# Optimization experiments

Measured on AMD Instinct MI355X. Metric: run time of the kernel, lower is better.

## Reference

```python
import jax, jax.numpy as jnp
import numpy as np

D = 1024  # input_dim


def setup_inputs() -> dict:
    key = jax.random.key(0)
    ks = jax.random.split(key, 7)
    s = 1.0 / np.sqrt(D)
    x = jax.random.normal(ks[0], (4, 2048, D), dtype=jnp.float32)
    Wq = jax.random.uniform(ks[1], (D, D), jnp.float32, -s, s)
    bq = jax.random.uniform(ks[2], (D,), jnp.float32, -s, s)
    Wk = jax.random.uniform(ks[3], (D, D), jnp.float32, -s, s)
    bk = jax.random.uniform(ks[4], (D,), jnp.float32, -s, s)
    Wv = jax.random.uniform(ks[5], (D, D), jnp.float32, -s, s)
    bv = jax.random.uniform(ks[6], (D,), jnp.float32, -s, s)
    return {"x": x, "Wq": Wq, "bq": bq, "Wk": Wk, "bk": bk, "Wv": Wv, "bv": bv}


def reference(x, Wq, bq, Wk, bk, Wv, bv):
    # nn.Linear: x @ W.T + b
    q = jnp.einsum('bsd,ed->bse', x, Wq) + bq
    k = jnp.einsum('bsd,ed->bse', x, Wk) + bk
    v = jnp.einsum('bsd,ed->bse', x, Wv) + bv
    scale = 1.0 / jnp.sqrt(jnp.asarray(x.shape[-1], x.dtype))
    scores = jnp.einsum('bqe,bke->bqk', q, k) * scale  # [B,S,S]
    weights = jax.nn.softmax(scores, axis=-1)
    return jnp.einsum('bqk,bke->bqe', weights, v)
```

## Files before the change

kernel.cpp:

```cpp
#include <hip/hip_runtime.h>
#include <hip/hip_bf16.h>
#include <stdint.h>


typedef float f32x4 __attribute__((ext_vector_type(4)));
typedef short s16x8 __attribute__((ext_vector_type(8)));

__device__ __forceinline__ uint16_t f2bf(float f) {
    uint32_t u = __float_as_uint(f);
    u += 0x7fffu + ((u >> 16) & 1u);
    return (uint16_t)(u >> 16);
}

#define GLOAD16(gp, lp)                                                  \
    __builtin_amdgcn_global_load_lds(                                    \
        (const __attribute__((address_space(1))) uint32_t*)(gp),         \
        (__attribute__((address_space(3))) uint32_t*)(lp), 16, 0, 0)


__global__ __launch_bounds__(256, 2) void proj_qkv(
    const uint16_t* __restrict__ xb, const uint16_t* __restrict__ wqb,
    const uint16_t* __restrict__ wkb, const uint16_t* __restrict__ wvb,
    const float* __restrict__ bq, const float* __restrict__ bk,
    const float* __restrict__ bv,
    uint16_t* __restrict__ qb, uint16_t* __restrict__ kb,
    uint16_t* __restrict__ vtb)
{
    __shared__ __attribute__((aligned(16))) uint16_t As[128 * 64];
    __shared__ __attribute__((aligned(16))) uint16_t Bs1[128 * 64];
    __shared__ __attribute__((aligned(16))) uint16_t Bs2[128 * 64];

    const int id = blockIdx.x;
    const bool qk = id < 512;

    const int t = threadIdx.x;
    const int wave = t >> 6, lane = t & 63;
    const int wm = (wave >> 1) * 64, wn = (wave & 1) * 64;
    const int lr = lane & 15;
    const int lr7 = lr & 7;

    long long row0, col0;
    const uint16_t *A, *B1, *B2;
    if (qk) {
        row0 = (long long)(id >> 3) * 128;
        col0 = (long long)(id & 7) * 128;
        A = xb; B1 = wqb; B2 = wkb;
    } else {
        const int vid = id - 512;
        row0 = (long long)(vid & 7) * 128;
        col0 = (long long)(vid >> 3) * 128;
        A = wvb; B1 = xb; B2 = nullptr;
    }

    const uint16_t* gA[4]; const uint16_t* gB1[4]; const uint16_t* gB2[4];
    uint16_t* lA[4]; uint16_t* lB1[4]; uint16_t* lB2[4];
#pragma unroll
    for (int p = 0; p < 4; ++p) {
        const int cs = p * 256 + wave * 64 + lane;
        const int rr = cs >> 3;
        const int kc = ((cs & 7) ^ (rr & 7)) * 8;
        gA[p]  = A  + (row0 + rr) * 1024 + kc;
        gB1[p] = B1 + (col0 + rr) * 1024 + kc;
        if (qk) gB2[p] = B2 + (col0 + rr) * 1024 + kc;
        lA[p]  = As  + (p * 256 + wave * 64) * 8;
        lB1[p] = Bs1 + (p * 256 + wave * 64) * 8;
        lB2[p] = Bs2 + (p * 256 + wave * 64) * 8;
    }

    f32x4 acc1[4][4] = {};
    f32x4 acc2[4][4] = {};

    for (int k0 = 0; k0 < 1024; k0 += 64) {
#pragma unroll
        for (int p = 0; p < 4; ++p) GLOAD16(gA[p] + k0, lA[p]);
#pragma unroll
        for (int p = 0; p < 4; ++p) GLOAD16(gB1[p] + k0, lB1[p]);
        if (qk) {
#pragma unroll
            for (int p = 0; p < 4; ++p) GLOAD16(gB2[p] + k0, lB2[p]);
        }
        __syncthreads();

#pragma unroll
        for (int kk = 0; kk < 2; ++kk) {
            const int lka = ((kk * 4 + (lane >> 4)) ^ lr7) * 8;
            s16x8 a[4], b[4];
#pragma unroll
            for (int i = 0; i < 4; ++i)
                a[i] = *(const s16x8*)(As + (wm + i * 16 + lr) * 64 + lka);
#pragma unroll
            for (int j = 0; j < 4; ++j)
                b[j] = *(const s16x8*)(Bs1 + (wn + j * 16 + lr) * 64 + lka);
#pragma unroll
            for (int i = 0; i < 4; ++i)
#pragma unroll
                for (int j = 0; j < 4; ++j)
                    acc1[i][j] = __builtin_amdgcn_mfma_f32_16x16x32_bf16(
                        a[i], b[j], acc1[i][j], 0, 0, 0);
            if (qk) {
#pragma unroll
                for (int j = 0; j < 4; ++j)
                    b[j] = *(const s16x8*)(Bs2 + (wn + j * 16 + lr) * 64 + lka);
#pragma unroll
                for (int i = 0; i < 4; ++i)
#pragma unroll
                    for (int j = 0; j < 4; ++j)
                        acc2[i][j] = __builtin_amdgcn_mfma_f32_16x16x32_bf16(
                            a[i], b[j], acc2[i][j], 0, 0, 0);
            }
        }
        __syncthreads();
    }

    const int rbase = wm + (lane >> 4) * 4;
    const int cbase = wn + lr;
    if (qk) {
#pragma unroll
        for (int i = 0; i < 4; ++i)
#pragma unroll
            for (int rr = 0; rr < 4; ++rr) {
                const long long row = row0 + rbase + i * 16 + rr;
#pragma unroll
                for (int j = 0; j < 4; ++j) {
                    const long long col = col0 + cbase + j * 16;
                    qb[row * 1024 + col] = f2bf((acc1[i][j][rr] + bq[col]) * 0.03125f);
                    kb[row * 1024 + col] = f2bf(acc2[i][j][rr] + bk[col]);
                }
            }
    } else {
#pragma unroll
        for (int i = 0; i < 4; ++i)
#pragma unroll
            for (int rr = 0; rr < 4; ++rr) {
                const long long row = row0 + rbase + i * 16 + rr;
                const float bb = bv[row];
#pragma unroll
                for (int j = 0; j < 4; ++j) {
                    const long long col = col0 + cbase + j * 16;
                    vtb[row * 8192 + col] = f2bf(acc1[i][j][rr] + bb);
                }
            }
    }
}

__global__ __launch_bounds__(256, 2) void gemm_exp(
    const uint16_t* __restrict__ Q, const uint16_t* __restrict__ Km,
    uint16_t* __restrict__ P, float* __restrict__ sums)
{
    __shared__ __attribute__((aligned(16))) uint16_t As[128 * 64];
    __shared__ __attribute__((aligned(16))) uint16_t Bs1[128 * 64];
    __shared__ __attribute__((aligned(16))) uint16_t Bs2[128 * 64];

    const int z = blockIdx.z;
    const uint16_t* Ab = Q  + (long long)z * 2048 * 1024;
    const uint16_t* Bb = Km + (long long)z * 2048 * 1024;
    uint16_t* Cb = P + (long long)z * 2048 * 2048;
    float* ax = sums + (long long)z * 2048;

    const int t = threadIdx.x;
    const int wave = t >> 6, lane = t & 63;
    const int wm = (wave >> 1) * 64, wn = (wave & 1) * 64;
    const int lr = lane & 15;
    const int lr7 = lr & 7;
    const long long row0  = (long long)blockIdx.x * 128;
    const long long col0a = (long long)blockIdx.y * 256;
    const long long col0b = col0a + 128;

    const uint16_t* gA[4]; const uint16_t* gB1[4]; const uint16_t* gB2[4];
    uint16_t* lA[4]; uint16_t* lB1[4]; uint16_t* lB2[4];
#pragma unroll
    for (int p = 0; p < 4; ++p) {
        const int cs = p * 256 + wave * 64 + lane;
        const int rr = cs >> 3;
        const int kc = ((cs & 7) ^ (rr & 7)) * 8;
        gA[p]  = Ab + (row0  + rr) * 1024 + kc;
        gB1[p] = Bb + (col0a + rr) * 1024 + kc;
        gB2[p] = Bb + (col0b + rr) * 1024 + kc;
        lA[p]  = As  + (p * 256 + wave * 64) * 8;
        lB1[p] = Bs1 + (p * 256 + wave * 64) * 8;
        lB2[p] = Bs2 + (p * 256 + wave * 64) * 8;
    }

    f32x4 acc1[4][4] = {};
    f32x4 acc2[4][4] = {};

    for (int k0 = 0; k0 < 1024; k0 += 64) {
#pragma unroll
        for (int p = 0; p < 4; ++p) GLOAD16(gA[p] + k0, lA[p]);
#pragma unroll
        for (int p = 0; p < 4; ++p) GLOAD16(gB1[p] + k0, lB1[p]);
#pragma unroll
        for (int p = 0; p < 4; ++p) GLOAD16(gB2[p] + k0, lB2[p]);
        __syncthreads();

#pragma unroll
        for (int kk = 0; kk < 2; ++kk) {
            const int lka = ((kk * 4 + (lane >> 4)) ^ lr7) * 8;
            s16x8 a[4], b[4];
#pragma unroll
            for (int i = 0; i < 4; ++i)
                a[i] = *(const s16x8*)(As + (wm + i * 16 + lr) * 64 + lka);
#pragma unroll
            for (int j = 0; j < 4; ++j)
                b[j] = *(const s16x8*)(Bs1 + (wn + j * 16 + lr) * 64 + lka);
#pragma unroll
            for (int i = 0; i < 4; ++i)
#pragma unroll
                for (int j = 0; j < 4; ++j)
                    acc1[i][j] = __builtin_amdgcn_mfma_f32_16x16x32_bf16(
                        a[i], b[j], acc1[i][j], 0, 0, 0);
#pragma unroll
            for (int j = 0; j < 4; ++j)
                b[j] = *(const s16x8*)(Bs2 + (wn + j * 16 + lr) * 64 + lka);
#pragma unroll
            for (int i = 0; i < 4; ++i)
#pragma unroll
                for (int j = 0; j < 4; ++j)
                    acc2[i][j] = __builtin_amdgcn_mfma_f32_16x16x32_bf16(
                        a[i], b[j], acc2[i][j], 0, 0, 0);
        }
        __syncthreads();
    }

    const int rbase = wm + (lane >> 4) * 4;
    const int cbase = wn + lr;
#pragma unroll
    for (int i = 0; i < 4; ++i)
#pragma unroll
        for (int rr = 0; rr < 4; ++rr) {
            const long long row = row0 + rbase + i * 16 + rr;
            float s = 0.f;
#pragma unroll
            for (int j = 0; j < 4; ++j) {
                const long long ca = col0a + cbase + j * 16;
                const long long cb2 = col0b + cbase + j * 16;
                const float va = __expf(acc1[i][j][rr]);
                const float vb = __expf(acc2[i][j][rr]);
                Cb[row * 2048 + ca]  = f2bf(va);
                Cb[row * 2048 + cb2] = f2bf(vb);
                s += va + vb;
            }
            s += __shfl_xor(s, 1);
            s += __shfl_xor(s, 2);
            s += __shfl_xor(s, 4);
            s += __shfl_xor(s, 8);
            if (lr == 0) atomicAdd(&ax[row], s);
        }
}

__global__ __launch_bounds__(256, 2) void gemm_pv(
    const uint16_t* __restrict__ P, const uint16_t* __restrict__ Vt,
    float* __restrict__ Out, const float* __restrict__ sums)
{
    __shared__ __attribute__((aligned(16))) uint16_t As[128 * 64];
    __shared__ __attribute__((aligned(16))) uint16_t Bs[128 * 64];

    const int z = blockIdx.z;
    const uint16_t* Ab = P + (long long)z * 2048 * 2048;
    const uint16_t* Bb = Vt + (long long)z * 2048;
    float* Cb = Out + (long long)z * 2048 * 1024;
    const float* ax = sums + (long long)z * 2048;

    const int t = threadIdx.x;
    const int wave = t >> 6, lane = t & 63;
    const int wm = (wave >> 1) * 64, wn = (wave & 1) * 64;
    const int lr = lane & 15;
    const int lr7 = lr & 7;
    const long long row0 = (long long)blockIdx.x * 128;
    const long long col0 = (long long)blockIdx.y * 128;

    const uint16_t* gA[4]; const uint16_t* gB[4];
    uint16_t* lA[4]; uint16_t* lB[4];
#pragma unroll
    for (int p = 0; p < 4; ++p) {
        const int cs = p * 256 + wave * 64 + lane;
        const int rr = cs >> 3;
        const int kc = ((cs & 7) ^ (rr & 7)) * 8;
        gA[p] = Ab + (row0 + rr) * 2048 + kc;
        gB[p] = Bb + (col0 + rr) * 8192 + kc;
        lA[p] = As + (p * 256 + wave * 64) * 8;
        lB[p] = Bs + (p * 256 + wave * 64) * 8;
    }

    f32x4 acc[4][4] = {};

    for (int k0 = 0; k0 < 2048; k0 += 64) {
#pragma unroll
        for (int p = 0; p < 4; ++p) GLOAD16(gA[p] + k0, lA[p]);
#pragma unroll
        for (int p = 0; p < 4; ++p) GLOAD16(gB[p] + k0, lB[p]);
        __syncthreads();

#pragma unroll
        for (int kk = 0; kk < 2; ++kk) {
            const int lka = ((kk * 4 + (lane >> 4)) ^ lr7) * 8;
            s16x8 a[4], b[4];
#pragma unroll
            for (int i = 0; i < 4; ++i)
                a[i] = *(const s16x8*)(As + (wm + i * 16 + lr) * 64 + lka);
#pragma unroll
            for (int j = 0; j < 4; ++j)
                b[j] = *(const s16x8*)(Bs + (wn + j * 16 + lr) * 64 + lka);
#pragma unroll
            for (int i = 0; i < 4; ++i)
#pragma unroll
                for (int j = 0; j < 4; ++j)
                    acc[i][j] = __builtin_amdgcn_mfma_f32_16x16x32_bf16(
                        a[i], b[j], acc[i][j], 0, 0, 0);
        }
        __syncthreads();
    }

    const int rbase = wm + (lane >> 4) * 4;
    const int cbase = wn + lr;
#pragma unroll
    for (int i = 0; i < 4; ++i)
#pragma unroll
        for (int rr = 0; rr < 4; ++rr) {
            const long long row = row0 + rbase + i * 16 + rr;
            const float linv = __builtin_amdgcn_rcpf(ax[row]);
#pragma unroll
            for (int j = 0; j < 4; ++j) {
                const long long col = col0 + cbase + j * 16;
                Cb[row * 1024 + col] = acc[i][j][rr] * linv;
            }
        }
}

__global__ void cast_all(const float* __restrict__ x, const float* __restrict__ Wq,
                         const float* __restrict__ Wk, const float* __restrict__ Wv,
                         uint16_t* __restrict__ xb, uint16_t* __restrict__ wqb,
                         uint16_t* __restrict__ wkb, uint16_t* __restrict__ wvb,
                         float* __restrict__ sums) {
    const int b = blockIdx.x;
    const float* in;
    uint16_t* out;
    int i;
    if (b < 8192)       { in = x;  out = xb;  i = b * 256 + threadIdx.x; }
    else if (b < 9216)  { in = Wq; out = wqb; i = (b - 8192) * 256 + threadIdx.x; }
    else if (b < 10240) { in = Wk; out = wkb; i = (b - 9216) * 256 + threadIdx.x; }
    else if (b < 11264) { in = Wv; out = wvb; i = (b - 10240) * 256 + threadIdx.x; }
    else {
        int j = (b - 11264) * 256 + threadIdx.x;
        ((float4*)sums)[j] = make_float4(0.f, 0.f, 0.f, 0.f);
        return;
    }
    float4 v = ((const float4*)in)[i];
    ushort4 o = make_ushort4(f2bf(v.x), f2bf(v.y), f2bf(v.z), f2bf(v.w));
    ((ushort4*)out)[i] = o;
}

extern "C" void kernel_launch(void* const* d_in, const int* in_sizes, int n_in,
                              void* d_out, int out_size, void* d_ws, size_t ws_size,
                              hipStream_t stream) {
    const float* x  = (const float*)d_in[0];
    const float* Wq = (const float*)d_in[1];
    const float* bq = (const float*)d_in[2];
    const float* Wk = (const float*)d_in[3];
    const float* bk = (const float*)d_in[4];
    const float* Wv = (const float*)d_in[5];
    const float* bv = (const float*)d_in[6];

    uint8_t* w = (uint8_t*)d_ws;
    uint16_t* xb  = (uint16_t*)w; w += (size_t)8192 * 1024 * 2;
    uint16_t* wqb = (uint16_t*)w; w += (size_t)1024 * 1024 * 2;
    uint16_t* wkb = (uint16_t*)w; w += (size_t)1024 * 1024 * 2;
    uint16_t* wvb = (uint16_t*)w; w += (size_t)1024 * 1024 * 2;
    uint16_t* qb  = (uint16_t*)w; w += (size_t)8192 * 1024 * 2;
    uint16_t* kb  = (uint16_t*)w; w += (size_t)8192 * 1024 * 2;
    uint16_t* vtb = (uint16_t*)w; w += (size_t)8192 * 1024 * 2;
    uint16_t* pb  = (uint16_t*)w; w += (size_t)4 * 2048 * 2048 * 2;
    float*    sums = (float*)w;  w += (size_t)8192 * 4;

    cast_all<<<dim3(11272), dim3(256), 0, stream>>>(x, Wq, Wk, Wv,
                                                    xb, wqb, wkb, wvb, sums);
    proj_qkv<<<dim3(1024), 256, 0, stream>>>(xb, wqb, wkb, wvb, bq, bk, bv,
                                             qb, kb, vtb);
    gemm_exp<<<dim3(16, 8, 4), 256, 0, stream>>>(qb, kb, pb, sums);
    gemm_pv<<<dim3(16, 8, 4), 256, 0, stream>>>(pb, vtb, (float*)d_out, sums);
}
```

Baseline: 234.6 us.

## Shrink proj K-tile, remap block order for L2 locality, raise occupancy bounds

The projection kernel's K-tile shrinks from 64 to 32, which halves its LDS use and changes the swizzle and load pattern, and its launch bound rises to 3 blocks per CU. The QK-exp and PV kernels switch to a 1D grid with a grouped block mapping, so neighbouring blocks share A and B tiles in L2, and their launch bounds rise to 3 and 4. The aim is more resident blocks to hide latency and fewer redundant global fetches. The cost is twice as many barriers per K step in the projection, and possible register spilling under the tighter bounds.

```diff
diff --git a/kernel.cpp b/kernel.cpp
--- a/kernel.cpp
+++ b/kernel.cpp
@@ -18,7 +18,7 @@
         (__attribute__((address_space(3))) uint32_t*)(lp), 16, 0, 0)
 
 
-__global__ __launch_bounds__(256, 2) void proj_qkv(
+__global__ __launch_bounds__(256, 3) void proj_qkv(
     const uint16_t* __restrict__ xb, const uint16_t* __restrict__ wqb,
     const uint16_t* __restrict__ wkb, const uint16_t* __restrict__ wvb,
     const float* __restrict__ bq, const float* __restrict__ bk,
@@ -26,9 +26,9 @@
     uint16_t* __restrict__ qb, uint16_t* __restrict__ kb,
     uint16_t* __restrict__ vtb)
 {
-    __shared__ __attribute__((aligned(16))) uint16_t As[128 * 64];
-    __shared__ __attribute__((aligned(16))) uint16_t Bs1[128 * 64];
-    __shared__ __attribute__((aligned(16))) uint16_t Bs2[128 * 64];
+    __shared__ __attribute__((aligned(16))) uint16_t As[128 * 32];
+    __shared__ __attribute__((aligned(16))) uint16_t Bs1[128 * 32];
+    __shared__ __attribute__((aligned(16))) uint16_t Bs2[128 * 32];
 
     const int id = blockIdx.x;
     const bool qk = id < 512;
@@ -37,77 +37,80 @@
     const int wave = t >> 6, lane = t & 63;
     const int wm = (wave >> 1) * 64, wn = (wave & 1) * 64;
     const int lr = lane & 15;
-    const int lr7 = lr & 7;
 
     long long row0, col0;
     const uint16_t *A, *B1, *B2;
     if (qk) {
-        row0 = (long long)(id >> 3) * 128;
-        col0 = (long long)(id & 7) * 128;
+        const int m = ((id >> 6) << 3) + (id & 7);
+        const int n = (id >> 3) & 7;
+        row0 = (long long)m * 128;
+        col0 = (long long)n * 128;
         A = xb; B1 = wqb; B2 = wkb;
     } else {
         const int vid = id - 512;
-        row0 = (long long)(vid & 7) * 128;
-        col0 = (long long)(vid >> 3) * 128;
+        const int m = (vid >> 3) & 7;
+        const int n = (vid & 7) + ((vid >> 6) << 3);
+        row0 = (long long)m * 128;
+        col0 = (long long)n * 128;
         A = wvb; B1 = xb; B2 = nullptr;
     }
 
-    const uint16_t* gA[4]; const uint16_t* gB1[4]; const uint16_t* gB2[4];
-    uint16_t* lA[4]; uint16_t* lB1[4]; uint16_t* lB2[4];
-#pragma unroll
-    for (int p = 0; p < 4; ++p) {
-        const int cs = p * 256 + wave * 64 + lane;
-        const int rr = cs >> 3;
-        const int kc = ((cs & 7) ^ (rr & 7)) * 8;
-        gA[p]  = A  + (row0 + rr) * 1024 + kc;
-        gB1[p] = B1 + (col0 + rr) * 1024 + kc;
-        if (qk) gB2[p] = B2 + (col0 + rr) * 1024 + kc;
-        lA[p]  = As  + (p * 256 + wave * 64) * 8;
-        lB1[p] = Bs1 + (p * 256 + wave * 64) * 8;
-        lB2[p] = Bs2 + (p * 256 + wave * 64) * 8;
-    }
+    const int c0 = wave * 64 + lane;
+    const int c1 = c0 + 256;
+    const int kc0 = ((c0 & 3) ^ ((c0 >> 3) & 3)) * 8;
+    const int kc1 = ((c1 & 3) ^ ((c1 >> 3) & 3)) * 8;
+    const uint16_t* gA0  = A  + (row0 + (c0 >> 2)) * 1024 + kc0;
+    const uint16_t* gA1  = A  + (row0 + (c1 >> 2)) * 1024 + kc1;
+    const uint16_t* gB10 = B1 + (col0 + (c0 >> 2)) * 1024 + kc0;
+    const uint16_t* gB11 = B1 + (col0 + (c1 >> 2)) * 1024 + kc1;
+    const uint16_t* gB20 = qk ? B2 + (col0 + (c0 >> 2)) * 1024 + kc0 : nullptr;
+    const uint16_t* gB21 = qk ? B2 + (col0 + (c1 >> 2)) * 1024 + kc1 : nullptr;
+    uint16_t* lA0  = As  + wave * 512;
+    uint16_t* lA1  = As  + wave * 512 + 2048;
+    uint16_t* lB10 = Bs1 + wave * 512;
+    uint16_t* lB11 = Bs1 + wave * 512 + 2048;
+    uint16_t* lB20 = Bs2 + wave * 512;
+    uint16_t* lB21 = Bs2 + wave * 512 + 2048;
+
+    const int lka = (((lane >> 4) ^ ((lr >> 1) & 3))) * 8;
 
     f32x4 acc1[4][4] = {};
     f32x4 acc2[4][4] = {};
 
-    for (int k0 = 0; k0 < 1024; k0 += 64) {
-#pragma unroll
-        for (int p = 0; p < 4; ++p) GLOAD16(gA[p] + k0, lA[p]);
-#pragma unroll
-        for (int p = 0; p < 4; ++p) GLOAD16(gB1[p] + k0, lB1[p]);
+    for (int k0 = 0; k0 < 1024; k0 += 32) {
+        GLOAD16(gA0 + k0, lA0);
+        GLOAD16(gA1 + k0, lA1);
+        GLOAD16(gB10 + k0, lB10);
+        GLOAD16(gB11 + k0, lB11);
         if (qk) {
-#pragma unroll
-            for (int p = 0; p < 4; ++p) GLOAD16(gB2[p] + k0, lB2[p]);
-        }
-        __syncthreads();
-
-#pragma unroll
-        for (int kk = 0; kk < 2; ++kk) {
-            const int lka = ((kk * 4 + (lane >> 4)) ^ lr7) * 8;
-            s16x8 a[4], b[4];
-#pragma unroll
-            for (int i = 0; i < 4; ++i)
-                a[i] = *(const s16x8*)(As + (wm + i * 16 + lr) * 64 + lka);
-#pragma unroll
-            for (int j = 0; j < 4; ++j)
-                b[j] = *(const s16x8*)(Bs1 + (wn + j * 16 + lr) * 64 + lka);
+            GLOAD16(gB20 + k0, lB20);
+            GLOAD16(gB21 + k0, lB21);
+        }
+        __syncthreads();
+
+        s16x8 a[4], b[4];
+#pragma unroll
+        for (int i = 0; i < 4; ++i)
+            a[i] = *(const s16x8*)(As + (wm + i * 16 + lr) * 32 + lka);
+#pragma unroll
+        for (int j = 0; j < 4; ++j)
+            b[j] = *(const s16x8*)(Bs1 + (wn + j * 16 + lr) * 32 + lka);
+#pragma unroll
+        for (int i = 0; i < 4; ++i)
+#pragma unroll
+            for (int j = 0; j < 4; ++j)
+                acc1[i][j] = __builtin_amdgcn_mfma_f32_16x16x32_bf16(
+                    a[i], b[j], acc1[i][j], 0, 0, 0);
+        if (qk) {
+#pragma unroll
+            for (int j = 0; j < 4; ++j)
+                b[j] = *(const s16x8*)(Bs2 + (wn + j * 16 + lr) * 32 + lka);
 #pragma unroll
             for (int i = 0; i < 4; ++i)
 #pragma unroll
                 for (int j = 0; j < 4; ++j)
-                    acc1[i][j] = __builtin_amdgcn_mfma_f32_16x16x32_bf16(
-                        a[i], b[j], acc1[i][j], 0, 0, 0);
-            if (qk) {
-#pragma unroll
-                for (int j = 0; j < 4; ++j)
-                    b[j] = *(const s16x8*)(Bs2 + (wn + j * 16 + lr) * 64 + lka);
-#pragma unroll
-                for (int i = 0; i < 4; ++i)
-#pragma unroll
-                    for (int j = 0; j < 4; ++j)
-                        acc2[i][j] = __builtin_amdgcn_mfma_f32_16x16x32_bf16(
-                            a[i], b[j], acc2[i][j], 0, 0, 0);
-            }
+                    acc2[i][j] = __builtin_amdgcn_mfma_f32_16x16x32_bf16(
+                        a[i], b[j], acc2[i][j], 0, 0, 0);
         }
         __syncthreads();
     }
@@ -143,7 +146,7 @@
     }
 }
 
-__global__ __launch_bounds__(256, 2) void gemm_exp(
+__global__ __launch_bounds__(256, 3) void gemm_exp(
     const uint16_t* __restrict__ Q, const uint16_t* __restrict__ Km,
     uint16_t* __restrict__ P, float* __restrict__ sums)
 {
@@ -151,7 +154,11 @@
     __shared__ __attribute__((aligned(16))) uint16_t Bs1[128 * 64];
     __shared__ __attribute__((aligned(16))) uint16_t Bs2[128 * 64];
 
-    const int z = blockIdx.z;
+    const int id = blockIdx.x;
+    const int g = (id & 7) + ((id >> 6) << 3);
+    const int y = (id >> 3) & 7;
+    const int xblk = g & 15, z = g >> 4;
+
     const uint16_t* Ab = Q  + (long long)z * 2048 * 1024;
     const uint16_t* Bb = Km + (long long)z * 2048 * 1024;
     uint16_t* Cb = P + (long long)z * 2048 * 2048;
@@ -162,8 +169,8 @@
     const int wm = (wave >> 1) * 64, wn = (wave & 1) * 64;
     const int lr = lane & 15;
     const int lr7 = lr & 7;
-    const long long row0  = (long long)blockIdx.x * 128;
-    const long long col0a = (long long)blockIdx.y * 256;
+    const long long row0  = (long long)xblk * 128;
+    const long long col0a = (long long)y * 256;
     const long long col0b = col0a + 128;
 
     const uint16_t* gA[4]; const uint16_t* gB1[4]; const uint16_t* gB2[4];
@@ -248,14 +255,18 @@
         }
 }
 
-__global__ __launch_bounds__(256, 2) void gemm_pv(
+__global__ __launch_bounds__(256, 4) void gemm_pv(
     const uint16_t* __restrict__ P, const uint16_t* __restrict__ Vt,
     float* __restrict__ Out, const float* __restrict__ sums)
 {
     __shared__ __attribute__((aligned(16))) uint16_t As[128 * 64];
     __shared__ __attribute__((aligned(16))) uint16_t Bs[128 * 64];
 
-    const int z = blockIdx.z;
+    const int id = blockIdx.x;
+    const int g = (id & 7) + ((id >> 6) << 3);
+    const int y = (id >> 3) & 7;
+    const int xblk = g & 15, z = g >> 4;
+
     const uint16_t* Ab = P + (long long)z * 2048 * 2048;
     const uint16_t* Bb = Vt + (long long)z * 2048;
     float* Cb = Out + (long long)z * 2048 * 1024;
@@ -266,8 +277,8 @@
     const int wm = (wave >> 1) * 64, wn = (wave & 1) * 64;
     const int lr = lane & 15;
     const int lr7 = lr & 7;
-    const long long row0 = (long long)blockIdx.x * 128;
-    const long long col0 = (long long)blockIdx.y * 128;
+    const long long row0 = (long long)xblk * 128;
+    const long long col0 = (long long)y * 128;
 
     const uint16_t* gA[4]; const uint16_t* gB[4];
     uint16_t* lA[4]; uint16_t* lB[4];
@@ -376,6 +387,6 @@
                                                     xb, wqb, wkb, wvb, sums);
     proj_qkv<<<dim3(1024), 256, 0, stream>>>(xb, wqb, wkb, wvb, bq, bk, bv,
                                              qb, kb, vtb);
-    gemm_exp<<<dim3(16, 8, 4), 256, 0, stream>>>(qb, kb, pb, sums);
-    gemm_pv<<<dim3(16, 8, 4), 256, 0, stream>>>(pb, vtb, (float*)d_out, sums);
-}
+    gemm_exp<<<dim3(512), 256, 0, stream>>>(qb, kb, pb, sums);
+    gemm_pv<<<dim3(512), 256, 0, stream>>>(pb, vtb, (float*)d_out, sums);
+}
```

Measured after the change: 376.7 us. +60.6%, slower.

## Balance QKV projection blocks by giving V blocks two output tiles and interleaving

Applied to the files above, without the earlier changes.

The V-projection blocks previously computed one 128x128 tile while Q/K blocks computed two, which left the grid unbalanced. Now each V block computes two adjacent column tiles (256 columns of V^T), so every block does the same amount of MFMA work, the grid shrinks from 1024 to 768 blocks, and Q/K and V blocks are interleaved in a 2:1 pattern. This is meant to remove tail imbalance and improve CU load distribution. In exchange, every block now holds two accumulator sets, and the interleaving changes L2 locality of x and weight reuse.

```diff
diff --git a/kernel.cpp b/kernel.cpp
--- a/kernel.cpp
+++ b/kernel.cpp
@@ -31,7 +31,9 @@
     __shared__ __attribute__((aligned(16))) uint16_t Bs2[128 * 64];
 
     const int id = blockIdx.x;
-    const bool qk = id < 512;
+    const int g3 = id / 3;
+    const int r3 = id - g3 * 3;
+    const bool qk = r3 < 2;
 
     const int t = threadIdx.x;
     const int wave = t >> 6, lane = t & 63;
@@ -39,17 +41,19 @@
     const int lr = lane & 15;
     const int lr7 = lr & 7;
 
-    long long row0, col0;
+    long long row0, col0a, col0b;
     const uint16_t *A, *B1, *B2;
     if (qk) {
-        row0 = (long long)(id >> 3) * 128;
-        col0 = (long long)(id & 7) * 128;
+        const int qkid = g3 * 2 + r3;
+        row0  = (long long)(qkid >> 3) * 128;
+        col0a = (long long)(qkid & 7) * 128;
+        col0b = col0a;
         A = xb; B1 = wqb; B2 = wkb;
     } else {
-        const int vid = id - 512;
-        row0 = (long long)(vid & 7) * 128;
-        col0 = (long long)(vid >> 3) * 128;
-        A = wvb; B1 = xb; B2 = nullptr;
+        row0  = (long long)(g3 >> 5) * 128;
+        col0a = (long long)(g3 & 31) * 256;
+        col0b = col0a + 128;
+        A = wvb; B1 = xb; B2 = xb;
     }
 
     const uint16_t* gA[4]; const uint16_t* gB1[4]; const uint16_t* gB2[4];
@@ -59,9 +63,9 @@
         const int cs = p * 256 + wave * 64 + lane;
         const int rr = cs >> 3;
         const int kc = ((cs & 7) ^ (rr & 7)) * 8;
-        gA[p]  = A  + (row0 + rr) * 1024 + kc;
-        gB1[p] = B1 + (col0 + rr) * 1024 + kc;
-        if (qk) gB2[p] = B2 + (col0 + rr) * 1024 + kc;
+        gA[p]  = A  + (row0  + rr) * 1024 + kc;
+        gB1[p] = B1 + (col0a + rr) * 1024 + kc;
+        gB2[p] = B2 + (col0b + rr) * 1024 + kc;
         lA[p]  = As  + (p * 256 + wave * 64) * 8;
         lB1[p] = Bs1 + (p * 256 + wave * 64) * 8;
         lB2[p] = Bs2 + (p * 256 + wave * 64) * 8;
@@ -75,10 +79,8 @@
         for (int p = 0; p < 4; ++p) GLOAD16(gA[p] + k0, lA[p]);
 #pragma unroll
         for (int p = 0; p < 4; ++p) GLOAD16(gB1[p] + k0, lB1[p]);
-        if (qk) {
-#pragma unroll
-            for (int p = 0; p < 4; ++p) GLOAD16(gB2[p] + k0, lB2[p]);
-        }
+#pragma unroll
+        for (int p = 0; p < 4; ++p) GLOAD16(gB2[p] + k0, lB2[p]);
         __syncthreads();
 
 #pragma unroll
@@ -97,17 +99,15 @@
                 for (int j = 0; j < 4; ++j)
                     acc1[i][j] = __builtin_amdgcn_mfma_f32_16x16x32_bf16(
                         a[i], b[j], acc1[i][j], 0, 0, 0);
-            if (qk) {
-#pragma unroll
-                for (int j = 0; j < 4; ++j)
-                    b[j] = *(const s16x8*)(Bs2 + (wn + j * 16 + lr) * 64 + lka);
-#pragma unroll
-                for (int i = 0; i < 4; ++i)
-#pragma unroll
-                    for (int j = 0; j < 4; ++j)
-                        acc2[i][j] = __builtin_amdgcn_mfma_f32_16x16x32_bf16(
-                            a[i], b[j], acc2[i][j], 0, 0, 0);
-            }
+#pragma unroll
+            for (int j = 0; j < 4; ++j)
+                b[j] = *(const s16x8*)(Bs2 + (wn + j * 16 + lr) * 64 + lka);
+#pragma unroll
+            for (int i = 0; i < 4; ++i)
+#pragma unroll
+                for (int j = 0; j < 4; ++j)
+                    acc2[i][j] = __builtin_amdgcn_mfma_f32_16x16x32_bf16(
+                        a[i], b[j], acc2[i][j], 0, 0, 0);
         }
         __syncthreads();
     }
@@ -122,7 +122,7 @@
                 const long long row = row0 + rbase + i * 16 + rr;
 #pragma unroll
                 for (int j = 0; j < 4; ++j) {
-                    const long long col = col0 + cbase + j * 16;
+                    const long long col = col0a + cbase + j * 16;
                     qb[row * 1024 + col] = f2bf((acc1[i][j][rr] + bq[col]) * 0.03125f);
                     kb[row * 1024 + col] = f2bf(acc2[i][j][rr] + bk[col]);
                 }
@@ -136,8 +136,10 @@
                 const float bb = bv[row];
 #pragma unroll
                 for (int j = 0; j < 4; ++j) {
-                    const long long col = col0 + cbase + j * 16;
-                    vtb[row * 8192 + col] = f2bf(acc1[i][j][rr] + bb);
+                    const long long ca  = col0a + cbase + j * 16;
+                    const long long cb2 = col0b + cbase + j * 16;
+                    vtb[row * 8192 + ca]  = f2bf(acc1[i][j][rr] + bb);
+                    vtb[row * 8192 + cb2] = f2bf(acc2[i][j][rr] + bb);
                 }
             }
     }
@@ -374,8 +376,8 @@
 
     cast_all<<<dim3(11272), dim3(256), 0, stream>>>(x, Wq, Wk, Wv,
                                                     xb, wqb, wkb, wvb, sums);
-    proj_qkv<<<dim3(1024), 256, 0, stream>>>(xb, wqb, wkb, wvb, bq, bk, bv,
-                                             qb, kb, vtb);
+    proj_qkv<<<dim3(768), 256, 0, stream>>>(xb, wqb, wkb, wvb, bq, bk, bv,
+                                            qb, kb, vtb);
     gemm_exp<<<dim3(16, 8, 4), 256, 0, stream>>>(qb, kb, pb, sums);
     gemm_pv<<<dim3(16, 8, 4), 256, 0, stream>>>(pb, vtb, (float*)d_out, sums);
 }
```

Result: no change. 236.3 us (+0.7%).
